# Optimization experiments

Measured on AMD Instinct MI355X. Metric: run time of the kernel, lower is better.

## Reference

```python
import jax, jax.numpy as jnp
import numpy as np
from math import sqrt

KEY_DIM = 128
VALUE_DIM = 128
SUMMARY_DIM = 128
QUESTION_NUM = 10000
CONCEPT_NUM = 64
B = 128
S = 128


def setup_inputs() -> dict:
    key = jax.random.key(0)
    ks = jax.random.split(key, 24)
    stdev = 1.0 / sqrt(CONCEPT_NUM + KEY_DIM)

    def lin_w(k, out_f, in_f):
        bound = 1.0 / sqrt(in_f)
        return jax.random.uniform(k, (out_f, in_f), jnp.float32, -bound, bound)

    def lin_b(k, out_f, in_f):
        bound = 1.0 / sqrt(in_f)
        return jax.random.uniform(k, (out_f,), jnp.float32, -bound, bound)

    q_emb = jax.random.normal(ks[0], (QUESTION_NUM + 1, KEY_DIM), jnp.float32)
    q_emb = q_emb.at[0].set(0.0)  # padding_idx = 0
    i_emb = jax.random.normal(ks[1], (2 * QUESTION_NUM + 1, VALUE_DIM), jnp.float32)
    i_emb = i_emb.at[0].set(0.0)

    inp = {
        "right_input": jax.random.randint(ks[2], (B, S), 0, 2 * QUESTION_NUM + 1),
        "wrong_input": jax.random.randint(ks[3], (B, S), 0, 2 * QUESTION_NUM + 1),
        "target_id": jax.random.randint(ks[4], (B,), 0, QUESTION_NUM + 1),
        "q_emb": q_emb,
        "i_emb": i_emb,
        "key_W": lin_w(ks[5], CONCEPT_NUM, KEY_DIM),  # no bias
        "erase_W": lin_w(ks[6], VALUE_DIM, VALUE_DIM),
        "erase_b": lin_b(ks[7], VALUE_DIM, VALUE_DIM),
        "add_W": lin_w(ks[8], VALUE_DIM, VALUE_DIM),
        "add_b": lin_b(ks[9], VALUE_DIM, VALUE_DIM),
        "rsum_W": lin_w(ks[10], SUMMARY_DIM, VALUE_DIM + KEY_DIM),
        "rsum_b": lin_b(ks[11], SUMMARY_DIM, VALUE_DIM + KEY_DIM),
        "wsum_W": lin_w(ks[12], SUMMARY_DIM, VALUE_DIM + KEY_DIM),
        "wsum_b": lin_b(ks[13], SUMMARY_DIM, VALUE_DIM + KEY_DIM),
        "succ_W": lin_w(ks[14], 1, SUMMARY_DIM),
        "succ_b": lin_b(ks[15], 1, SUMMARY_DIM),
        "fail_W": lin_w(ks[16], 1, SUMMARY_DIM),
        "fail_b": lin_b(ks[17], 1, SUMMARY_DIM),
        "diff_W": lin_w(ks[18], 1, KEY_DIM),
        "diff_b": lin_b(ks[19], 1, KEY_DIM),
        "right_mem_init": jax.random.uniform(ks[20], (VALUE_DIM, CONCEPT_NUM), jnp.float32, -stdev, stdev),
        "wrong_mem_init": jax.random.uniform(ks[21], (VALUE_DIM, CONCEPT_NUM), jnp.float32, -stdev, stdev),
    }
    return inp


def reference(right_input, wrong_input, target_id, q_emb, i_emb, key_W,
              erase_W, erase_b, add_W, add_b, rsum_W, rsum_b, wsum_W, wsum_b,
              succ_W, succ_b, fail_W, fail_b, diff_W, diff_b,
              right_mem_init, wrong_mem_init):
    Q = (i_emb.shape[0] - 1) // 2
    batch = right_input.shape[0]

    def corr(qid):  # (B,) -> (B, C) correlation weights
        return jax.nn.softmax(q_emb[qid] @ key_W.T, axis=-1)

    def update(mem, inter):
        # mem: (B, V, C); inter: (B,) interaction ids
        vec = i_emb[inter]                                  # (B, V)
        e = jax.nn.sigmoid(vec @ erase_W.T + erase_b)       # (B, V)
        a = jnp.tanh(vec @ add_W.T + add_b)                 # (B, V)
        qid = inter - Q * (inter > Q).astype(inter.dtype)
        w = corr(qid)                                       # (B, C)
        # erase/add are outer products w (x) e, w (x) a -> (B, V, C)
        return mem * (1.0 - e[:, :, None] * w[:, None, :]) + a[:, :, None] * w[:, None, :]

    def step(carry, xs):
        rm, wm = carry
        ri, wi = xs
        return (update(rm, ri), update(wm, wi)), None

    rm0 = jnp.broadcast_to(right_mem_init, (batch,) + right_mem_init.shape)
    wm0 = jnp.broadcast_to(wrong_mem_init, (batch,) + wrong_mem_init.shape)
    (rm, wm), _ = jax.lax.scan(step, (rm0, wm0), (right_input.T, wrong_input.T))

    qv = q_emb[target_id]                                   # (B, K)
    w_t = corr(target_id)                                   # (B, C)
    right_read = jnp.einsum('bvc,bc->bv', rm, w_t)          # (B, V)
    wrong_read = jnp.einsum('bvc,bc->bv', wm, w_t)

    r_sum = jnp.tanh(jnp.concatenate([right_read, qv], axis=-1) @ rsum_W.T + rsum_b)
    w_sum = jnp.tanh(jnp.concatenate([wrong_read, qv], axis=-1) @ wsum_W.T + wsum_b)

    success_level = jnp.tanh(r_sum @ succ_W.T + succ_b)     # (B, 1)
    failure_level = jnp.tanh(w_sum @ fail_W.T + fail_b)     # (B, 1)
    difficulty_level = jnp.tanh(qv @ diff_W.T + diff_b)     # (B, 1)

    success_count = jnp.sum(jnp.clip(right_input, 0, 1)).astype(jnp.float32)
    failure_count = jnp.sum(jnp.clip(wrong_input, 0, 1)).astype(jnp.float32)

    out = (success_level * jax.nn.sigmoid(success_count)
           + failure_level * jax.nn.sigmoid(failure_count)
           - difficulty_level * 2.0)
    return out
```

## Files before the change

### kernel.cpp

```cpp
#include <hip/hip_runtime.h>
#include <hip/hip_bf16.h>

#define BB 128
#define SS 128
#define VD 128
#define CN 64
#define KD 128
#define QN 10000

typedef __attribute__((ext_vector_type(8))) short bf16x8;
typedef __attribute__((ext_vector_type(4))) float f32x4;
typedef __attribute__((ext_vector_type(2))) float f32x2;

__device__ __forceinline__ float bflo(unsigned int u) { return __uint_as_float(u << 16); }
__device__ __forceinline__ float bfhi(unsigned int u) { return __uint_as_float(u & 0xffff0000u); }
__device__ __forceinline__ unsigned short f2bf(float f) {
    unsigned int x = __float_as_uint(f);
    return (unsigned short)((x + 0x7fffu + ((x >> 16) & 1u)) >> 16);
}
__device__ __forceinline__ unsigned int pk2(float lo, float hi) {
    return (unsigned int)f2bf(lo) | ((unsigned int)f2bf(hi) << 16);
}
__device__ __forceinline__ float fast_tanh(float x) {
    float e = __expf(2.0f * x);
    return 1.0f - 2.0f / (e + 1.0f);
}
__device__ __forceinline__ float fast_sig(float x) {
    return 1.0f / (1.0f + __expf(-x));
}
__device__ __forceinline__ f32x2 pk_fma(f32x2 a, f32x2 b, f32x2 c) {
    f32x2 d;
    asm("v_pk_fma_f32 %0, %1, %2, %3" : "=v"(d) : "v"(a), "v"(b), "v"(c));
    return d;
}
__device__ __forceinline__ f32x2 pk_nfma(f32x2 a, f32x2 b, f32x2 c) {
    f32x2 d;
    asm("v_pk_fma_f32 %0, %1, %2, %3 neg_lo:[1,0,0] neg_hi:[1,0,0]"
        : "=v"(d) : "v"(a), "v"(b), "v"(c));
    return d;
}

__global__ __launch_bounds__(256) void k_wcnt(
    const float* __restrict__ erase_W, const float* __restrict__ add_W,
    const float* __restrict__ key_W, unsigned short* __restrict__ Bfrag,
    const int* __restrict__ ri, const int* __restrict__ wi, float* __restrict__ sig)
{
    if (blockIdx.x < 20) {
        const int bid = blockIdx.x * 4 + (threadIdx.x >> 6);
        const int l = threadIdx.x & 63;
        const int n = (bid >> 2) * 16 + (l & 15);
        const int k0 = (bid & 3) * 32 + (l >> 4) * 8;
        const float* src;
        if (n < 128)      src = erase_W + (size_t)n * KD + k0;
        else if (n < 256) src = add_W + (size_t)(n - 128) * KD + k0;
        else              src = key_W + (size_t)(n - 256) * KD + k0;
        float4 fa = ((const float4*)src)[0];
        float4 fb = ((const float4*)src)[1];
        uint4 o = make_uint4(pk2(fa.x, fa.y), pk2(fa.z, fa.w), pk2(fb.x, fb.y), pk2(fb.z, fb.w));
        *(uint4*)(Bfrag + ((size_t)bid * 64 + l) * 8) = o;
    } else {
        __shared__ int sr_s[4], sw_s[4];
        const int t = threadIdx.x;
        const int4* r4 = (const int4*)ri;
        const int4* w4 = (const int4*)wi;
        int sr = 0, sw = 0;
        #pragma unroll 4
        for (int p = 0; p < 16; ++p) {
            int4 a = r4[p * 256 + t];
            int4 b = w4[p * 256 + t];
            sr += (a.x >= 1) + (a.y >= 1) + (a.z >= 1) + (a.w >= 1);
            sw += (b.x >= 1) + (b.y >= 1) + (b.z >= 1) + (b.w >= 1);
        }
        for (int off = 1; off < 64; off <<= 1) { sr += __shfl_xor(sr, off); sw += __shfl_xor(sw, off); }
        int wid = t >> 6;
        if ((t & 63) == 0) { sr_s[wid] = sr; sw_s[wid] = sw; }
        __syncthreads();
        if (t == 0) {
            int SR = sr_s[0]+sr_s[1]+sr_s[2]+sr_s[3];
            int SW = sw_s[0]+sw_s[1]+sw_s[2]+sw_s[3];
            sig[0] = 1.0f / (1.0f + __expf(-(float)SR));
            sig[1] = 1.0f / (1.0f + __expf(-(float)SW));
        }
    }
}

__global__ __launch_bounds__(512, 2) void k_chain(
    const int* __restrict__ ri, const int* __restrict__ wi, const int* __restrict__ tgt,
    const float* __restrict__ q_emb, const float* __restrict__ i_emb,
    const float* __restrict__ key_W,
    const float* __restrict__ erase_b, const float* __restrict__ add_b,
    const unsigned short* __restrict__ Bfrag,
    const float* __restrict__ rmem0, const float* __restrict__ wmem0,
    float* __restrict__ readbuf)
{
    __shared__ __align__(16) unsigned int lds_ea[SS * VD];
    __shared__ __align__(16) char xab[32 * 1024];
    __shared__ __align__(16) float logits[SS * 68];
    __shared__ __align__(16) unsigned short lds_w[SS * CN];
    __shared__ float q_t[KD];
    __shared__ float logit_t[CN];
    __shared__ float wt_lds[CN];
    __shared__ int qid_s[SS], ir_s[SS];
    __shared__ float psum[8 * 64];

    const int t = threadIdx.x;
    const int lane = t & 63;
    const int w = t >> 6;
    const int chain = blockIdx.x;
    const int m = chain >> 7;
    const int b = chain & 127;

    if (t < SS) {
        int inter = (m == 0 ? ri : wi)[b * SS + t];
        ir_s[t] = inter;
        qid_s[t] = (inter > QN) ? inter - QN : inter;
        q_t[t] = q_emb[(size_t)tgt[b] * KD + t];
    }
    __syncthreads();

    {
        const int r0 = t >> 3, o = t & 7;
        #pragma unroll
        for (int h = 0; h < 2; ++h) {
            const int r = r0 + h * 64;
            const float* src = q_emb + (size_t)qid_s[r] * KD + o * 16;
            float4 f0 = ((const float4*)src)[0];
            float4 f1 = ((const float4*)src)[1];
            float4 f2 = ((const float4*)src)[2];
            float4 f3 = ((const float4*)src)[3];
            const int bb = r * 256 + o * 32;
            const int sw = (r & 7) << 4;
            *(uint4*)(xab + (bb ^ sw))        = make_uint4(pk2(f0.x,f0.y), pk2(f0.z,f0.w), pk2(f1.x,f1.y), pk2(f1.z,f1.w));
            *(uint4*)(xab + ((bb + 16) ^ sw)) = make_uint4(pk2(f2.x,f2.y), pk2(f2.z,f2.w), pk2(f3.x,f3.y), pk2(f3.z,f3.w));
        }
        const int c = t >> 3, oct = t & 7;
        const float* kw = key_W + (size_t)c * KD + oct * 16;
        float s = 0.f;
        #pragma unroll
        for (int i = 0; i < 16; ++i) s = fmaf(kw[i], q_t[oct * 16 + i], s);
        s += __shfl_xor(s, 1); s += __shfl_xor(s, 2); s += __shfl_xor(s, 4);
        if (oct == 0) logit_t[c] = s;
    }
    __syncthreads();

    const int rowl = lane & 15;
    const int kb16 = (lane >> 4) * 16;
    const int rb4 = (lane >> 4) * 4;

    {
        if (w == 0) {
            float x = logit_t[lane];
            float mx = x;
            #pragma unroll
            for (int off = 1; off < 64; off <<= 1) mx = fmaxf(mx, __shfl_xor(mx, off));
            float e = __expf(x - mx);
            float ssum = e;
            #pragma unroll
            for (int off = 1; off < 64; off <<= 1) ssum += __shfl_xor(ssum, off);
            wt_lds[lane] = e / ssum;
        }
        bf16x8 afQ[4];
        const int row = w * 16 + rowl;
        #pragma unroll
        for (int kt = 0; kt < 4; ++kt)
            afQ[kt] = *(const bf16x8*)(xab + ((row * 256 + kt * 64 + kb16) ^ ((row & 7) << 4)));
        #pragma unroll
        for (int nt = 0; nt < 4; ++nt) {
            f32x4 acc = {0.f,0.f,0.f,0.f};
            #pragma unroll
            for (int kt = 0; kt < 4; ++kt) {
                bf16x8 bf = *(const bf16x8*)(Bfrag + ((size_t)((16 + nt) * 4 + kt) * 64 + lane) * 8);
                acc = __builtin_amdgcn_mfma_f32_16x16x32_bf16(afQ[kt], bf, acc, 0, 0, 0);
            }
            #pragma unroll
            for (int rr = 0; rr < 4; ++rr)
                logits[(w * 16 + rb4 + rr) * 68 + nt * 16 + rowl] = acc[rr];
        }
    }
    __syncthreads();

    {
        const int r0 = t >> 3, o = t & 7;
        uint4 xi[2][2];
        #pragma unroll
        for (int h = 0; h < 2; ++h) {
            const int r = r0 + h * 64;
            const float* src = i_emb + (size_t)ir_s[r] * KD + o * 16;
            float4 f0 = ((const float4*)src)[0];
            float4 f1 = ((const float4*)src)[1];
            float4 f2 = ((const float4*)src)[2];
            float4 f3 = ((const float4*)src)[3];
            xi[h][0] = make_uint4(pk2(f0.x,f0.y), pk2(f0.z,f0.w), pk2(f1.x,f1.y), pk2(f1.z,f1.w));
            xi[h][1] = make_uint4(pk2(f2.x,f2.y), pk2(f2.z,f2.w), pk2(f3.x,f3.y), pk2(f3.z,f3.w));
        }

        const int rr = t >> 2, q4 = t & 3;
        const float* L = logits + rr * 68 + q4 * 16;
        float4 va = ((const float4*)L)[0];
        float4 vb = ((const float4*)L)[1];
        float4 vc = ((const float4*)L)[2];
        float4 vd = ((const float4*)L)[3];
        float mx = fmaxf(fmaxf(fmaxf(va.x, va.y), fmaxf(va.z, va.w)),
                         fmaxf(fmaxf(vb.x, vb.y), fmaxf(vb.z, vb.w)));
        mx = fmaxf(mx, fmaxf(fmaxf(fmaxf(vc.x, vc.y), fmaxf(vc.z, vc.w)),
                             fmaxf(fmaxf(vd.x, vd.y), fmaxf(vd.z, vd.w))));
        mx = fmaxf(mx, __shfl_xor(mx, 1));
        mx = fmaxf(mx, __shfl_xor(mx, 2));
        float ex[16];
        ex[0] = __expf(va.x - mx); ex[1] = __expf(va.y - mx); ex[2] = __expf(va.z - mx); ex[3] = __expf(va.w - mx);
        ex[4] = __expf(vb.x - mx); ex[5] = __expf(vb.y - mx); ex[6] = __expf(vb.z - mx); ex[7] = __expf(vb.w - mx);
        ex[8] = __expf(vc.x - mx); ex[9] = __expf(vc.y - mx); ex[10] = __expf(vc.z - mx); ex[11] = __expf(vc.w - mx);
        ex[12] = __expf(vd.x - mx); ex[13] = __expf(vd.y - mx); ex[14] = __expf(vd.z - mx); ex[15] = __expf(vd.w - mx);
        float s = 0.f;
        #pragma unroll
        for (int i = 0; i < 16; ++i) s += ex[i];
        s += __shfl_xor(s, 1);
        s += __shfl_xor(s, 2);
        float inv = 1.0f / s;
        uint4 o0 = make_uint4(pk2(ex[0]*inv, ex[1]*inv), pk2(ex[2]*inv, ex[3]*inv),
                              pk2(ex[4]*inv, ex[5]*inv), pk2(ex[6]*inv, ex[7]*inv));
        uint4 o1 = make_uint4(pk2(ex[8]*inv, ex[9]*inv), pk2(ex[10]*inv, ex[11]*inv),
                              pk2(ex[12]*inv, ex[13]*inv), pk2(ex[14]*inv, ex[15]*inv));
        *(uint4*)(lds_w + rr * CN + q4 * 16)     = o0;
        *(uint4*)(lds_w + rr * CN + q4 * 16 + 8) = o1;

        #pragma unroll
        for (int h = 0; h < 2; ++h) {
            const int r = r0 + h * 64;
            const int bb = r * 256 + o * 32;
            const int sw = (r & 7) << 4;
            *(uint4*)(xab + (bb ^ sw))        = xi[h][0];
            *(uint4*)(xab + ((bb + 16) ^ sw)) = xi[h][1];
        }
    }
    __syncthreads();

    {
        bf16x8 afI[4];
        const int row = w * 16 + rowl;
        #pragma unroll
        for (int kt = 0; kt < 4; ++kt)
            afI[kt] = *(const bf16x8*)(xab + ((row * 256 + kt * 64 + kb16) ^ ((row & 7) << 4)));
        #pragma unroll
        for (int ci = 0; ci < 8; ++ci) {
            f32x4 ae = {0.f,0.f,0.f,0.f}, aa = {0.f,0.f,0.f,0.f};
            #pragma unroll
            for (int kt = 0; kt < 4; ++kt) {
                bf16x8 be = *(const bf16x8*)(Bfrag + ((size_t)(ci * 4 + kt) * 64 + lane) * 8);
                bf16x8 ba = *(const bf16x8*)(Bfrag + ((size_t)((8 + ci) * 4 + kt) * 64 + lane) * 8);
                ae = __builtin_amdgcn_mfma_f32_16x16x32_bf16(afI[kt], be, ae, 0, 0, 0);
                aa = __builtin_amdgcn_mfma_f32_16x16x32_bf16(afI[kt], ba, aa, 0, 0, 0);
            }
            const int cc = ci * 16 + rowl;
            const float bvE = erase_b[cc];
            const float bvA = add_b[cc];
            #pragma unroll
            for (int rr = 0; rr < 4; ++rr) {
                float e = fast_sig(ae[rr] + bvE);
                float a = fast_tanh(aa[rr] + bvA);
                lds_ea[(w * 16 + rb4 + rr) * VD + cc] = pk2(e, a);
            }
        }
    }

    const int vhalf = w & 1;
    const int cq = w >> 1;
    const int vg = lane >> 2;
    const int cg = lane & 3;
    const int v0 = vhalf * 64 + vg * 4;
    const int c0 = cq * 16 + cg * 4;
    const float* minit = (m == 0) ? rmem0 : wmem0;
    f32x2 mA[4], mB[4];
    #pragma unroll
    for (int j = 0; j < 4; ++j) {
        float4 mi = *(const float4*)(minit + (v0 + j) * CN + c0);
        mA[j].x = mi.x; mA[j].y = mi.y;
        mB[j].x = mi.z; mB[j].y = mi.w;
    }
    __syncthreads();

    for (int so = 0; so < 16; ++so) {
        const unsigned int* eap = lds_ea + (so * 8) * VD + v0;
        const unsigned short* wp = lds_w + (so * 8) * CN + c0;
        #pragma unroll
        for (int kk = 0; kk < 8; ++kk) {
            uint4 ea = *(const uint4*)(eap + kk * VD);
            uint2 wu = *(const uint2*)(wp + kk * CN);
            f32x2 wA; wA.x = bflo(wu.x); wA.y = bfhi(wu.x);
            f32x2 wB; wB.x = bflo(wu.y); wB.y = bfhi(wu.y);
            unsigned int eu[4] = { ea.x, ea.y, ea.z, ea.w };
            #pragma unroll
            for (int j = 0; j < 4; ++j) {
                float e = bflo(eu[j]), a = bfhi(eu[j]);
                f32x2 ev; ev.x = e; ev.y = e;
                f32x2 av; av.x = a; av.y = a;
                f32x2 g;
                g = pk_nfma(ev, mA[j], av);
                mA[j] = pk_fma(wA, g, mA[j]);
                g = pk_nfma(ev, mB[j], av);
                mB[j] = pk_fma(wB, g, mB[j]);
            }
        }
    }

    {
        float4 wt = *(const float4*)(wt_lds + c0);
        float p[4];
        #pragma unroll
        for (int j = 0; j < 4; ++j) {
            float x = mA[j].x * wt.x;
            x = fmaf(mA[j].y, wt.y, x);
            x = fmaf(mB[j].x, wt.z, x);
            x = fmaf(mB[j].y, wt.w, x);
            p[j] = x;
        }
        #pragma unroll
        for (int j = 0; j < 4; ++j) {
            p[j] += __shfl_xor(p[j], 1);
            p[j] += __shfl_xor(p[j], 2);
        }
        if (cg == 0) {
            #pragma unroll
            for (int j = 0; j < 4; ++j) psum[w * 64 + vg * 4 + j] = p[j];
        }
    }
    __syncthreads();
    if (t < 128) {
        const int vh = t >> 6, vl = t & 63;
        float s = psum[(0 * 2 + vh) * 64 + vl] + psum[(1 * 2 + vh) * 64 + vl]
                + psum[(2 * 2 + vh) * 64 + vl] + psum[(3 * 2 + vh) * 64 + vl];
        readbuf[(size_t)chain * VD + t] = s;
    }
}

__global__ __launch_bounds__(256) void k_head(
    const float* __restrict__ readbuf, const int* __restrict__ tgt,
    const float* __restrict__ q_emb,
    const float* __restrict__ rsum_W, const float* __restrict__ rsum_b,
    const float* __restrict__ wsum_W, const float* __restrict__ wsum_b,
    const float* __restrict__ succ_W, const float* __restrict__ succ_b,
    const float* __restrict__ fail_W, const float* __restrict__ fail_b,
    const float* __restrict__ diff_W, const float* __restrict__ diff_b,
    const float* __restrict__ sig, float* __restrict__ out)
{
    __shared__ float xr[256], xw[256];
    __shared__ float part[2][128];
    __shared__ float red_s[6];
    const int t = threadIdx.x;
    const int j = t & 127;
    const int h = t >> 7;
    const int b = blockIdx.x;
    if (h == 0) {
        int tid_ = tgt[b];
        float qv = q_emb[(size_t)tid_ * KD + j];
        xr[j]       = readbuf[(size_t)b * VD + j];
        xr[128 + j] = qv;
        xw[j]       = readbuf[(size_t)(BB + b) * VD + j];
        xw[128 + j] = qv;
    }
    __syncthreads();

    float rs = (h == 0) ? rsum_b[j] : 0.0f;
    float wv = (h == 0) ? wsum_b[j] : 0.0f;
    const float* rw = rsum_W + (size_t)j * 256 + h * 128;
    const float* ww = wsum_W + (size_t)j * 256 + h * 128;
    const float* xrp = xr + h * 128;
    const float* xwp = xw + h * 128;
    #pragma unroll 4
    for (int k = 0; k < 128; ++k) {
        rs = fmaf(rw[k], xrp[k], rs);
        wv = fmaf(ww[k], xwp[k], wv);
    }
    if (h == 1) { part[0][j] = rs; part[1][j] = wv; }
    __syncthreads();
    if (h == 0) {
        rs += part[0][j];
        wv += part[1][j];
        float r_sum = fast_tanh(rs), w_sum = fast_tanh(wv);
        float qv = xr[128 + j];
        float ps = r_sum * succ_W[j];
        float pf = w_sum * fail_W[j];
        float pd = qv    * diff_W[j];
        for (int off = 1; off < 64; off <<= 1) {
            ps += __shfl_xor(ps, off);
            pf += __shfl_xor(pf, off);
            pd += __shfl_xor(pd, off);
        }
        int wid = j >> 6;
        if ((j & 63) == 0) { red_s[wid*3+0] = ps; red_s[wid*3+1] = pf; red_s[wid*3+2] = pd; }
    }
    __syncthreads();
    if (t == 0) {
        float Ps = red_s[0] + red_s[3];
        float Pf = red_s[1] + red_s[4];
        float Pd = red_s[2] + red_s[5];
        float succ = fast_tanh(Ps + succ_b[0]);
        float fail = fast_tanh(Pf + fail_b[0]);
        float diff = fast_tanh(Pd + diff_b[0]);
        out[b] = succ * sig[0] + fail * sig[1] - 2.0f * diff;
    }
}

extern "C" void kernel_launch(void* const* d_in, const int* in_sizes, int n_in,
                              void* d_out, int out_size, void* d_ws, size_t ws_size,
                              hipStream_t stream) {
    const int*   ri      = (const int*)d_in[0];
    const int*   wi      = (const int*)d_in[1];
    const int*   tgt     = (const int*)d_in[2];
    const float* q_emb   = (const float*)d_in[3];
    const float* i_emb   = (const float*)d_in[4];
    const float* key_W   = (const float*)d_in[5];
    const float* erase_W = (const float*)d_in[6];
    const float* erase_b = (const float*)d_in[7];
    const float* add_W   = (const float*)d_in[8];
    const float* add_b   = (const float*)d_in[9];
    const float* rsum_W  = (const float*)d_in[10];
    const float* rsum_b  = (const float*)d_in[11];
    const float* wsum_W  = (const float*)d_in[12];
    const float* wsum_b  = (const float*)d_in[13];
    const float* succ_W  = (const float*)d_in[14];
    const float* succ_b  = (const float*)d_in[15];
    const float* fail_W  = (const float*)d_in[16];
    const float* fail_b  = (const float*)d_in[17];
    const float* diff_W  = (const float*)d_in[18];
    const float* diff_b  = (const float*)d_in[19];
    const float* rmem0   = (const float*)d_in[20];
    const float* wmem0   = (const float*)d_in[21];

    char* ws = (char*)d_ws;
    float*          readbuf = (float*)(ws + 0);
    unsigned short* Bfrag   = (unsigned short*)(ws + 131072);
    float*          sig     = (float*)(ws + 212992);
    float*          out     = (float*)d_out;

    hipLaunchKernelGGL(k_wcnt, dim3(21), dim3(256), 0, stream,
        erase_W, add_W, key_W, Bfrag, ri, wi, sig);
    hipLaunchKernelGGL(k_chain, dim3(256), dim3(512), 0, stream,
        ri, wi, tgt, q_emb, i_emb, key_W, erase_b, add_b, Bfrag,
        rmem0, wmem0, readbuf);
    hipLaunchKernelGGL(k_head, dim3(128), dim3(256), 0, stream,
        readbuf, tgt, q_emb, rsum_W, rsum_b, wsum_W, wsum_b,
        succ_W, succ_b, fail_W, fail_b, diff_W, diff_b, sig, out);
}
```

Measured before the change: 52.95 us.

## Split memory recurrence across two thread groups using affine composition

Doubles the k_chain block to 1024 threads. The sequential erase/add scan over 128 steps is split into two halves. Group 0 runs the first 64 steps from the initial memory, and group 1 runs the last 64 steps as an affine map (a product of decay factors plus an offset) starting from zero. The halves are then combined through LDS, which halves the serial dependency chain. The MFMA and softmax phases are also redistributed across the extra waves. The cost is extra multiplies in the second half, higher register and LDS pressure, and lower occupancy per CU with 1024-thread blocks.

After: 55.43 us. +4.7%, slower.

```diff
diff --git a/kernel.cpp b/kernel.cpp
--- a/kernel.cpp
+++ b/kernel.cpp
@@ -84,7 +84,7 @@
     }
 }
 
-__global__ __launch_bounds__(512, 2) void k_chain(
+__global__ __launch_bounds__(1024, 4) void k_chain(
     const int* __restrict__ ri, const int* __restrict__ wi, const int* __restrict__ tgt,
     const float* __restrict__ q_emb, const float* __restrict__ i_emb,
     const float* __restrict__ key_W,
@@ -119,33 +119,32 @@
     __syncthreads();
 
     {
-        const int r0 = t >> 3, o = t & 7;
-        #pragma unroll
-        for (int h = 0; h < 2; ++h) {
-            const int r = r0 + h * 64;
-            const float* src = q_emb + (size_t)qid_s[r] * KD + o * 16;
-            float4 f0 = ((const float4*)src)[0];
-            float4 f1 = ((const float4*)src)[1];
-            float4 f2 = ((const float4*)src)[2];
-            float4 f3 = ((const float4*)src)[3];
-            const int bb = r * 256 + o * 32;
-            const int sw = (r & 7) << 4;
-            *(uint4*)(xab + (bb ^ sw))        = make_uint4(pk2(f0.x,f0.y), pk2(f0.z,f0.w), pk2(f1.x,f1.y), pk2(f1.z,f1.w));
-            *(uint4*)(xab + ((bb + 16) ^ sw)) = make_uint4(pk2(f2.x,f2.y), pk2(f2.z,f2.w), pk2(f3.x,f3.y), pk2(f3.z,f3.w));
-        }
-        const int c = t >> 3, oct = t & 7;
-        const float* kw = key_W + (size_t)c * KD + oct * 16;
-        float s = 0.f;
-        #pragma unroll
-        for (int i = 0; i < 16; ++i) s = fmaf(kw[i], q_t[oct * 16 + i], s);
-        s += __shfl_xor(s, 1); s += __shfl_xor(s, 2); s += __shfl_xor(s, 4);
-        if (oct == 0) logit_t[c] = s;
+        const int r = t >> 3, o = t & 7;
+        const float* src = q_emb + (size_t)qid_s[r] * KD + o * 16;
+        float4 f0 = ((const float4*)src)[0];
+        float4 f1 = ((const float4*)src)[1];
+        float4 f2 = ((const float4*)src)[2];
+        float4 f3 = ((const float4*)src)[3];
+        const int bb = r * 256 + o * 32;
+        const int sw = (r & 7) << 4;
+        *(uint4*)(xab + (bb ^ sw))        = make_uint4(pk2(f0.x,f0.y), pk2(f0.z,f0.w), pk2(f1.x,f1.y), pk2(f1.z,f1.w));
+        *(uint4*)(xab + ((bb + 16) ^ sw)) = make_uint4(pk2(f2.x,f2.y), pk2(f2.z,f2.w), pk2(f3.x,f3.y), pk2(f3.z,f3.w));
+        if (t < 512) {
+            const int c = t >> 3, oct = t & 7;
+            const float* kw = key_W + (size_t)c * KD + oct * 16;
+            float s = 0.f;
+            #pragma unroll
+            for (int i = 0; i < 16; ++i) s = fmaf(kw[i], q_t[oct * 16 + i], s);
+            s += __shfl_xor(s, 1); s += __shfl_xor(s, 2); s += __shfl_xor(s, 4);
+            if (oct == 0) logit_t[c] = s;
+        }
     }
     __syncthreads();
 
     const int rowl = lane & 15;
     const int kb16 = (lane >> 4) * 16;
     const int rb4 = (lane >> 4) * 4;
+    const int rt = w & 7;
 
     {
         if (w == 0) {
@@ -160,12 +159,14 @@
             wt_lds[lane] = e / ssum;
         }
         bf16x8 afQ[4];
-        const int row = w * 16 + rowl;
+        const int row = rt * 16 + rowl;
         #pragma unroll
         for (int kt = 0; kt < 4; ++kt)
             afQ[kt] = *(const bf16x8*)(xab + ((row * 256 + kt * 64 + kb16) ^ ((row & 7) << 4)));
-        #pragma unroll
-        for (int nt = 0; nt < 4; ++nt) {
+        const int nt0 = (w >> 3) * 2;
+        #pragma unroll
+        for (int ni = 0; ni < 2; ++ni) {
+            const int nt = nt0 + ni;
             f32x4 acc = {0.f,0.f,0.f,0.f};
             #pragma unroll
             for (int kt = 0; kt < 4; ++kt) {
@@ -174,75 +175,52 @@
             }
             #pragma unroll
             for (int rr = 0; rr < 4; ++rr)
-                logits[(w * 16 + rb4 + rr) * 68 + nt * 16 + rowl] = acc[rr];
+                logits[(rt * 16 + rb4 + rr) * 68 + nt * 16 + rowl] = acc[rr];
         }
     }
     __syncthreads();
 
     {
-        const int r0 = t >> 3, o = t & 7;
-        uint4 xi[2][2];
-        #pragma unroll
-        for (int h = 0; h < 2; ++h) {
-            const int r = r0 + h * 64;
-            const float* src = i_emb + (size_t)ir_s[r] * KD + o * 16;
-            float4 f0 = ((const float4*)src)[0];
-            float4 f1 = ((const float4*)src)[1];
-            float4 f2 = ((const float4*)src)[2];
-            float4 f3 = ((const float4*)src)[3];
-            xi[h][0] = make_uint4(pk2(f0.x,f0.y), pk2(f0.z,f0.w), pk2(f1.x,f1.y), pk2(f1.z,f1.w));
-            xi[h][1] = make_uint4(pk2(f2.x,f2.y), pk2(f2.z,f2.w), pk2(f3.x,f3.y), pk2(f3.z,f3.w));
-        }
-
-        const int rr = t >> 2, q4 = t & 3;
-        const float* L = logits + rr * 68 + q4 * 16;
+        const int rr = t >> 3, q = t & 7;
+        const float* L = logits + rr * 68 + q * 8;
         float4 va = ((const float4*)L)[0];
         float4 vb = ((const float4*)L)[1];
-        float4 vc = ((const float4*)L)[2];
-        float4 vd = ((const float4*)L)[3];
         float mx = fmaxf(fmaxf(fmaxf(va.x, va.y), fmaxf(va.z, va.w)),
                          fmaxf(fmaxf(vb.x, vb.y), fmaxf(vb.z, vb.w)));
-        mx = fmaxf(mx, fmaxf(fmaxf(fmaxf(vc.x, vc.y), fmaxf(vc.z, vc.w)),
-                             fmaxf(fmaxf(vd.x, vd.y), fmaxf(vd.z, vd.w))));
         mx = fmaxf(mx, __shfl_xor(mx, 1));
         mx = fmaxf(mx, __shfl_xor(mx, 2));
-        float ex[16];
-        ex[0] = __expf(va.x - mx); ex[1] = __expf(va.y - mx); ex[2] = __expf(va.z - mx); ex[3] = __expf(va.w - mx);
-        ex[4] = __expf(vb.x - mx); ex[5] = __expf(vb.y - mx); ex[6] = __expf(vb.z - mx); ex[7] = __expf(vb.w - mx);
-        ex[8] = __expf(vc.x - mx); ex[9] = __expf(vc.y - mx); ex[10] = __expf(vc.z - mx); ex[11] = __expf(vc.w - mx);
-        ex[12] = __expf(vd.x - mx); ex[13] = __expf(vd.y - mx); ex[14] = __expf(vd.z - mx); ex[15] = __expf(vd.w - mx);
-        float s = 0.f;
-        #pragma unroll
-        for (int i = 0; i < 16; ++i) s += ex[i];
-        s += __shfl_xor(s, 1);
-        s += __shfl_xor(s, 2);
+        mx = fmaxf(mx, __shfl_xor(mx, 4));
+        float e0 = __expf(va.x - mx), e1 = __expf(va.y - mx), e2 = __expf(va.z - mx), e3 = __expf(va.w - mx);
+        float e4 = __expf(vb.x - mx), e5 = __expf(vb.y - mx), e6 = __expf(vb.z - mx), e7 = __expf(vb.w - mx);
+        float s = e0 + e1 + e2 + e3 + e4 + e5 + e6 + e7;
+        s += __shfl_xor(s, 1); s += __shfl_xor(s, 2); s += __shfl_xor(s, 4);
         float inv = 1.0f / s;
-        uint4 o0 = make_uint4(pk2(ex[0]*inv, ex[1]*inv), pk2(ex[2]*inv, ex[3]*inv),
-                              pk2(ex[4]*inv, ex[5]*inv), pk2(ex[6]*inv, ex[7]*inv));
-        uint4 o1 = make_uint4(pk2(ex[8]*inv, ex[9]*inv), pk2(ex[10]*inv, ex[11]*inv),
-                              pk2(ex[12]*inv, ex[13]*inv), pk2(ex[14]*inv, ex[15]*inv));
-        *(uint4*)(lds_w + rr * CN + q4 * 16)     = o0;
-        *(uint4*)(lds_w + rr * CN + q4 * 16 + 8) = o1;
-
-        #pragma unroll
-        for (int h = 0; h < 2; ++h) {
-            const int r = r0 + h * 64;
-            const int bb = r * 256 + o * 32;
-            const int sw = (r & 7) << 4;
-            *(uint4*)(xab + (bb ^ sw))        = xi[h][0];
-            *(uint4*)(xab + ((bb + 16) ^ sw)) = xi[h][1];
-        }
+        uint4 o = make_uint4(pk2(e0*inv, e1*inv), pk2(e2*inv, e3*inv),
+                             pk2(e4*inv, e5*inv), pk2(e6*inv, e7*inv));
+        *(uint4*)(lds_w + rr * CN + q * 8) = o;
+
+        const float* src = i_emb + (size_t)ir_s[rr] * KD + q * 16;
+        float4 f0 = ((const float4*)src)[0];
+        float4 f1 = ((const float4*)src)[1];
+        float4 f2 = ((const float4*)src)[2];
+        float4 f3 = ((const float4*)src)[3];
+        const int bb = rr * 256 + q * 32;
+        const int sw = (rr & 7) << 4;
+        *(uint4*)(xab + (bb ^ sw))        = make_uint4(pk2(f0.x,f0.y), pk2(f0.z,f0.w), pk2(f1.x,f1.y), pk2(f1.z,f1.w));
+        *(uint4*)(xab + ((bb + 16) ^ sw)) = make_uint4(pk2(f2.x,f2.y), pk2(f2.z,f2.w), pk2(f3.x,f3.y), pk2(f3.z,f3.w));
     }
     __syncthreads();
 
     {
         bf16x8 afI[4];
-        const int row = w * 16 + rowl;
+        const int row = rt * 16 + rowl;
         #pragma unroll
         for (int kt = 0; kt < 4; ++kt)
             afI[kt] = *(const bf16x8*)(xab + ((row * 256 + kt * 64 + kb16) ^ ((row & 7) << 4)));
-        #pragma unroll
-        for (int ci = 0; ci < 8; ++ci) {
+        const int ci0 = (w >> 3) * 4;
+        #pragma unroll
+        for (int ii = 0; ii < 4; ++ii) {
+            const int ci = ci0 + ii;
             f32x4 ae = {0.f,0.f,0.f,0.f}, aa = {0.f,0.f,0.f,0.f};
             #pragma unroll
             for (int kt = 0; kt < 4; ++kt) {
@@ -258,60 +236,114 @@
             for (int rr = 0; rr < 4; ++rr) {
                 float e = fast_sig(ae[rr] + bvE);
                 float a = fast_tanh(aa[rr] + bvA);
-                lds_ea[(w * 16 + rb4 + rr) * VD + cc] = pk2(e, a);
+                lds_ea[(rt * 16 + rb4 + rr) * VD + cc] = pk2(e, a);
             }
         }
     }
 
-    const int vhalf = w & 1;
-    const int cq = w >> 1;
+    const int g  = w >> 3;
+    const int w2 = w & 7;
+    const int vhalf = w2 & 1;
+    const int cq = w2 >> 1;
     const int vg = lane >> 2;
     const int cg = lane & 3;
     const int v0 = vhalf * 64 + vg * 4;
     const int c0 = cq * 16 + cg * 4;
-    const float* minit = (m == 0) ? rmem0 : wmem0;
+
     f32x2 mA[4], mB[4];
-    #pragma unroll
-    for (int j = 0; j < 4; ++j) {
-        float4 mi = *(const float4*)(minit + (v0 + j) * CN + c0);
-        mA[j].x = mi.x; mA[j].y = mi.y;
-        mB[j].x = mi.z; mB[j].y = mi.w;
-    }
-    __syncthreads();
-
-    for (int so = 0; so < 16; ++so) {
-        const unsigned int* eap = lds_ea + (so * 8) * VD + v0;
-        const unsigned short* wp = lds_w + (so * 8) * CN + c0;
-        #pragma unroll
-        for (int kk = 0; kk < 8; ++kk) {
-            uint4 ea = *(const uint4*)(eap + kk * VD);
-            uint2 wu = *(const uint2*)(wp + kk * CN);
-            f32x2 wA; wA.x = bflo(wu.x); wA.y = bfhi(wu.x);
-            f32x2 wB; wB.x = bflo(wu.y); wB.y = bfhi(wu.y);
-            unsigned int eu[4] = { ea.x, ea.y, ea.z, ea.w };
-            #pragma unroll
-            for (int j = 0; j < 4; ++j) {
-                float e = bflo(eu[j]), a = bfhi(eu[j]);
-                f32x2 ev; ev.x = e; ev.y = e;
-                f32x2 av; av.x = a; av.y = a;
-                f32x2 g;
-                g = pk_nfma(ev, mA[j], av);
-                mA[j] = pk_fma(wA, g, mA[j]);
-                g = pk_nfma(ev, mB[j], av);
-                mB[j] = pk_fma(wB, g, mB[j]);
+    f32x2 DA[4], DB[4];
+    if (g == 0) {
+        const float* minit = (m == 0) ? rmem0 : wmem0;
+        #pragma unroll
+        for (int j = 0; j < 4; ++j) {
+            float4 mi = *(const float4*)(minit + (v0 + j) * CN + c0);
+            mA[j].x = mi.x; mA[j].y = mi.y;
+            mB[j].x = mi.z; mB[j].y = mi.w;
+        }
+    } else {
+        #pragma unroll
+        for (int j = 0; j < 4; ++j) {
+            mA[j].x = 0.f; mA[j].y = 0.f; mB[j].x = 0.f; mB[j].y = 0.f;
+            DA[j].x = 1.f; DA[j].y = 1.f; DB[j].x = 1.f; DB[j].y = 1.f;
+        }
+    }
+    __syncthreads();
+
+    if (g == 0) {
+        for (int so = 0; so < 8; ++so) {
+            const unsigned int* eap = lds_ea + (so * 8) * VD + v0;
+            const unsigned short* wp = lds_w + (so * 8) * CN + c0;
+            #pragma unroll
+            for (int kk = 0; kk < 8; ++kk) {
+                uint4 ea = *(const uint4*)(eap + kk * VD);
+                uint2 wu = *(const uint2*)(wp + kk * CN);
+                f32x2 wA; wA.x = bflo(wu.x); wA.y = bfhi(wu.x);
+                f32x2 wB; wB.x = bflo(wu.y); wB.y = bfhi(wu.y);
+                unsigned int eu[4] = { ea.x, ea.y, ea.z, ea.w };
+                #pragma unroll
+                for (int j = 0; j < 4; ++j) {
+                    float e = bflo(eu[j]), a = bfhi(eu[j]);
+                    f32x2 ev; ev.x = e; ev.y = e;
+                    f32x2 av; av.x = a; av.y = a;
+                    f32x2 gg;
+                    gg = pk_nfma(ev, mA[j], av);
+                    mA[j] = pk_fma(wA, gg, mA[j]);
+                    gg = pk_nfma(ev, mB[j], av);
+                    mB[j] = pk_fma(wB, gg, mB[j]);
+                }
             }
         }
-    }
-
-    {
+        float* mmid = logits;
+        #pragma unroll
+        for (int j = 0; j < 4; ++j) {
+            float4 f;
+            f.x = mA[j].x; f.y = mA[j].y; f.z = mB[j].x; f.w = mB[j].y;
+            *(float4*)(mmid + (v0 + j) * 68 + c0) = f;
+        }
+    } else {
+        f32x2 one; one.x = 1.f; one.y = 1.f;
+        for (int so = 8; so < 16; ++so) {
+            const unsigned int* eap = lds_ea + (so * 8) * VD + v0;
+            const unsigned short* wp = lds_w + (so * 8) * CN + c0;
+            #pragma unroll
+            for (int kk = 0; kk < 8; ++kk) {
+                uint4 ea = *(const uint4*)(eap + kk * VD);
+                uint2 wu = *(const uint2*)(wp + kk * CN);
+                f32x2 wA; wA.x = bflo(wu.x); wA.y = bfhi(wu.x);
+                f32x2 wB; wB.x = bflo(wu.y); wB.y = bfhi(wu.y);
+                unsigned int eu[4] = { ea.x, ea.y, ea.z, ea.w };
+                #pragma unroll
+                for (int j = 0; j < 4; ++j) {
+                    float e = bflo(eu[j]), a = bfhi(eu[j]);
+                    f32x2 ev; ev.x = e; ev.y = e;
+                    f32x2 av; av.x = a; av.y = a;
+                    f32x2 dA = pk_nfma(ev, wA, one);
+                    f32x2 dB = pk_nfma(ev, wB, one);
+                    DA[j] = DA[j] * dA;
+                    DB[j] = DB[j] * dB;
+                    mA[j] = pk_fma(mA[j], dA, av * wA);
+                    mB[j] = pk_fma(mB[j], dB, av * wB);
+                }
+            }
+        }
+    }
+    __syncthreads();
+
+    if (g == 1) {
+        const float* mmid = logits;
         float4 wt = *(const float4*)(wt_lds + c0);
         float p[4];
         #pragma unroll
         for (int j = 0; j < 4; ++j) {
-            float x = mA[j].x * wt.x;
-            x = fmaf(mA[j].y, wt.y, x);
-            x = fmaf(mB[j].x, wt.z, x);
-            x = fmaf(mB[j].y, wt.w, x);
+            float4 mi = *(const float4*)(mmid + (v0 + j) * 68 + c0);
+            f32x2 miA; miA.x = mi.x; miA.y = mi.y;
+            f32x2 miB; miB.x = mi.z; miB.y = mi.w;
+            f32x2 fA = pk_fma(DA[j], miA, mA[j]);
+            f32x2 fB = pk_fma(DB[j], miB, mB[j]);
+            float x = fA.x * wt.x;
+            x = fmaf(fA.y, wt.y, x);
+            x = fmaf(fB.x, wt.z, x);
+            x = fmaf(fB.y, wt.w, x);
             p[j] = x;
         }
         #pragma unroll
@@ -321,7 +353,7 @@
         }
         if (cg == 0) {
             #pragma unroll
-            for (int j = 0; j < 4; ++j) psum[w * 64 + vg * 4 + j] = p[j];
+            for (int j = 0; j < 4; ++j) psum[w2 * 64 + vg * 4 + j] = p[j];
         }
     }
     __syncthreads();
@@ -435,7 +467,7 @@
 
     hipLaunchKernelGGL(k_wcnt, dim3(21), dim3(256), 0, stream,
         erase_W, add_W, key_W, Bfrag, ri, wi, sig);
-    hipLaunchKernelGGL(k_chain, dim3(256), dim3(512), 0, stream,
+    hipLaunchKernelGGL(k_chain, dim3(256), dim3(1024), 0, stream,
         ri, wi, tgt, q_emb, i_emb, key_W, erase_b, add_b, Bfrag,
         rmem0, wmem0, readbuf);
     hipLaunchKernelGGL(k_head, dim3(128), dim3(256), 0, stream,
```

## Pre-convert embedding tables to bf16 and use hardware packed bf16 conversion

Applied to the files above, without the earlier changes.

Extends the weight-prep kernel with about 940 extra blocks that convert the whole q_emb and i_emb tables from fp32 to bf16 in workspace on every call. The chain kernel then gathers half-width bf16 rows instead of fp32 rows, and drops its per-element conversion work. The manual round-to-nearest packing is also replaced with the __float22bfloat162_rn intrinsic, which can map to a native packed convert instruction. The trade-off is that each call now streams the full tables (roughly 15 MB read and 7.7 MB written), and the chain kernel must wait for that pass. This may cost more than it saves on the gathered rows.

After: 54.53 us. 1.03x slower.

```diff
diff --git a/kernel.cpp b/kernel.cpp
--- a/kernel.cpp
+++ b/kernel.cpp
@@ -7,6 +7,9 @@
 #define CN 64
 #define KD 128
 #define QN 10000
+#define QSZ (10001 * 128)
+#define ISZ (20001 * 128)
+#define TOTE (QSZ + ISZ)
 
 typedef __attribute__((ext_vector_type(8))) short bf16x8;
 typedef __attribute__((ext_vector_type(4))) float f32x4;
@@ -14,12 +17,9 @@
 
 __device__ __forceinline__ float bflo(unsigned int u) { return __uint_as_float(u << 16); }
 __device__ __forceinline__ float bfhi(unsigned int u) { return __uint_as_float(u & 0xffff0000u); }
-__device__ __forceinline__ unsigned short f2bf(float f) {
-    unsigned int x = __float_as_uint(f);
-    return (unsigned short)((x + 0x7fffu + ((x >> 16) & 1u)) >> 16);
-}
-__device__ __forceinline__ unsigned int pk2(float lo, float hi) {
-    return (unsigned int)f2bf(lo) | ((unsigned int)f2bf(hi) << 16);
+__device__ __forceinline__ unsigned int cvtpk(float lo, float hi) {
+    __hip_bfloat162 h2 = __float22bfloat162_rn(make_float2(lo, hi));
+    unsigned int r; __builtin_memcpy(&r, &h2, 4); return r;
 }
 __device__ __forceinline__ float fast_tanh(float x) {
     float e = __expf(2.0f * x);
@@ -43,11 +43,14 @@
 __global__ __launch_bounds__(256) void k_wcnt(
     const float* __restrict__ erase_W, const float* __restrict__ add_W,
     const float* __restrict__ key_W, unsigned short* __restrict__ Bfrag,
-    const int* __restrict__ ri, const int* __restrict__ wi, float* __restrict__ sig)
+    const int* __restrict__ ri, const int* __restrict__ wi, float* __restrict__ sig,
+    const float* __restrict__ q_emb, const float* __restrict__ i_emb,
+    unsigned short* __restrict__ qbf, unsigned short* __restrict__ ibf)
 {
+    const int t = threadIdx.x;
     if (blockIdx.x < 20) {
-        const int bid = blockIdx.x * 4 + (threadIdx.x >> 6);
-        const int l = threadIdx.x & 63;
+        const int bid = blockIdx.x * 4 + (t >> 6);
+        const int l = t & 63;
         const int n = (bid >> 2) * 16 + (l & 15);
         const int k0 = (bid & 3) * 32 + (l >> 4) * 8;
         const float* src;
@@ -56,11 +59,10 @@
         else              src = key_W + (size_t)(n - 256) * KD + k0;
         float4 fa = ((const float4*)src)[0];
         float4 fb = ((const float4*)src)[1];
-        uint4 o = make_uint4(pk2(fa.x, fa.y), pk2(fa.z, fa.w), pk2(fb.x, fb.y), pk2(fb.z, fb.w));
+        uint4 o = make_uint4(cvtpk(fa.x, fa.y), cvtpk(fa.z, fa.w), cvtpk(fb.x, fb.y), cvtpk(fb.z, fb.w));
         *(uint4*)(Bfrag + ((size_t)bid * 64 + l) * 8) = o;
-    } else {
+    } else if (blockIdx.x == 20) {
         __shared__ int sr_s[4], sw_s[4];
-        const int t = threadIdx.x;
         const int4* r4 = (const int4*)ri;
         const int4* w4 = (const int4*)wi;
         int sr = 0, sw = 0;
@@ -81,12 +83,29 @@
             sig[0] = 1.0f / (1.0f + __expf(-(float)SR));
             sig[1] = 1.0f / (1.0f + __expf(-(float)SW));
         }
+    } else {
+        const int idx = (blockIdx.x - 21) * 256 + t;
+        const int base = idx * 16;
+        if (base < TOTE) {
+            const float* src; unsigned short* dst; int off;
+            if (base < QSZ) { src = q_emb; dst = qbf; off = base; }
+            else            { src = i_emb; dst = ibf; off = base - QSZ; }
+            float4 f0 = *(const float4*)(src + off);
+            float4 f1 = *(const float4*)(src + off + 4);
+            float4 f2 = *(const float4*)(src + off + 8);
+            float4 f3 = *(const float4*)(src + off + 12);
+            uint4 o0 = make_uint4(cvtpk(f0.x,f0.y), cvtpk(f0.z,f0.w), cvtpk(f1.x,f1.y), cvtpk(f1.z,f1.w));
+            uint4 o1 = make_uint4(cvtpk(f2.x,f2.y), cvtpk(f2.z,f2.w), cvtpk(f3.x,f3.y), cvtpk(f3.z,f3.w));
+            *(uint4*)(dst + off)     = o0;
+            *(uint4*)(dst + off + 8) = o1;
+        }
     }
 }
 
 __global__ __launch_bounds__(512, 2) void k_chain(
     const int* __restrict__ ri, const int* __restrict__ wi, const int* __restrict__ tgt,
-    const float* __restrict__ q_emb, const float* __restrict__ i_emb,
+    const float* __restrict__ q_emb,
+    const unsigned short* __restrict__ qbf, const unsigned short* __restrict__ ibf,
     const float* __restrict__ key_W,
     const float* __restrict__ erase_b, const float* __restrict__ add_b,
     const unsigned short* __restrict__ Bfrag,
@@ -123,15 +142,12 @@
         #pragma unroll
         for (int h = 0; h < 2; ++h) {
             const int r = r0 + h * 64;
-            const float* src = q_emb + (size_t)qid_s[r] * KD + o * 16;
-            float4 f0 = ((const float4*)src)[0];
-            float4 f1 = ((const float4*)src)[1];
-            float4 f2 = ((const float4*)src)[2];
-            float4 f3 = ((const float4*)src)[3];
+            const uint4* src = (const uint4*)(qbf + (size_t)qid_s[r] * KD) + o * 2;
+            uint4 s0 = src[0], s1 = src[1];
             const int bb = r * 256 + o * 32;
             const int sw = (r & 7) << 4;
-            *(uint4*)(xab + (bb ^ sw))        = make_uint4(pk2(f0.x,f0.y), pk2(f0.z,f0.w), pk2(f1.x,f1.y), pk2(f1.z,f1.w));
-            *(uint4*)(xab + ((bb + 16) ^ sw)) = make_uint4(pk2(f2.x,f2.y), pk2(f2.z,f2.w), pk2(f3.x,f3.y), pk2(f3.z,f3.w));
+            *(uint4*)(xab + (bb ^ sw))        = s0;
+            *(uint4*)(xab + ((bb + 16) ^ sw)) = s1;
         }
         const int c = t >> 3, oct = t & 7;
         const float* kw = key_W + (size_t)c * KD + oct * 16;
@@ -185,13 +201,9 @@
         #pragma unroll
         for (int h = 0; h < 2; ++h) {
             const int r = r0 + h * 64;
-            const float* src = i_emb + (size_t)ir_s[r] * KD + o * 16;
-            float4 f0 = ((const float4*)src)[0];
-            float4 f1 = ((const float4*)src)[1];
-            float4 f2 = ((const float4*)src)[2];
-            float4 f3 = ((const float4*)src)[3];
-            xi[h][0] = make_uint4(pk2(f0.x,f0.y), pk2(f0.z,f0.w), pk2(f1.x,f1.y), pk2(f1.z,f1.w));
-            xi[h][1] = make_uint4(pk2(f2.x,f2.y), pk2(f2.z,f2.w), pk2(f3.x,f3.y), pk2(f3.z,f3.w));
+            const uint4* src = (const uint4*)(ibf + (size_t)ir_s[r] * KD) + o * 2;
+            xi[h][0] = src[0];
+            xi[h][1] = src[1];
         }
 
         const int rr = t >> 2, q4 = t & 3;
@@ -217,10 +229,10 @@
         s += __shfl_xor(s, 1);
         s += __shfl_xor(s, 2);
         float inv = 1.0f / s;
-        uint4 o0 = make_uint4(pk2(ex[0]*inv, ex[1]*inv), pk2(ex[2]*inv, ex[3]*inv),
-                              pk2(ex[4]*inv, ex[5]*inv), pk2(ex[6]*inv, ex[7]*inv));
-        uint4 o1 = make_uint4(pk2(ex[8]*inv, ex[9]*inv), pk2(ex[10]*inv, ex[11]*inv),
-                              pk2(ex[12]*inv, ex[13]*inv), pk2(ex[14]*inv, ex[15]*inv));
+        uint4 o0 = make_uint4(cvtpk(ex[0]*inv, ex[1]*inv), cvtpk(ex[2]*inv, ex[3]*inv),
+                              cvtpk(ex[4]*inv, ex[5]*inv), cvtpk(ex[6]*inv, ex[7]*inv));
+        uint4 o1 = make_uint4(cvtpk(ex[8]*inv, ex[9]*inv), cvtpk(ex[10]*inv, ex[11]*inv),
+                              cvtpk(ex[12]*inv, ex[13]*inv), cvtpk(ex[14]*inv, ex[15]*inv));
         *(uint4*)(lds_w + rr * CN + q4 * 16)     = o0;
         *(uint4*)(lds_w + rr * CN + q4 * 16 + 8) = o1;
 
@@ -258,7 +270,7 @@
             for (int rr = 0; rr < 4; ++rr) {
                 float e = fast_sig(ae[rr] + bvE);
                 float a = fast_tanh(aa[rr] + bvA);
-                lds_ea[(w * 16 + rb4 + rr) * VD + cc] = pk2(e, a);
+                lds_ea[(w * 16 + rb4 + rr) * VD + cc] = cvtpk(e, a);
             }
         }
     }
@@ -431,12 +443,14 @@
     float*          readbuf = (float*)(ws + 0);
     unsigned short* Bfrag   = (unsigned short*)(ws + 131072);
     float*          sig     = (float*)(ws + 212992);
+    unsigned short* qbf     = (unsigned short*)(ws + 213504);
+    unsigned short* ibf     = (unsigned short*)(ws + 2773760);
     float*          out     = (float*)d_out;
 
-    hipLaunchKernelGGL(k_wcnt, dim3(21), dim3(256), 0, stream,
-        erase_W, add_W, key_W, Bfrag, ri, wi, sig);
+    hipLaunchKernelGGL(k_wcnt, dim3(959), dim3(256), 0, stream,
+        erase_W, add_W, key_W, Bfrag, ri, wi, sig, q_emb, i_emb, qbf, ibf);
     hipLaunchKernelGGL(k_chain, dim3(256), dim3(512), 0, stream,
-        ri, wi, tgt, q_emb, i_emb, key_W, erase_b, add_b, Bfrag,
+        ri, wi, tgt, q_emb, qbf, ibf, key_W, erase_b, add_b, Bfrag,
         rmem0, wmem0, readbuf);
     hipLaunchKernelGGL(k_head, dim3(128), dim3(256), 0, stream,
         readbuf, tgt, q_emb, rsum_W, rsum_b, wsum_W, wsum_b,
```
